# Performance work log

Hardware: AMD Instinct MI355X
Metric: run time of the kernel (lower is better)

## Reference

```python
import jax, jax.numpy as jnp
import numpy as np
import math

BN_EPS = 1e-5
BASES = [5, 4]
NH = 8    # num_heads
KD = 64   # key_dim = hidden_dim

def _bn(x, g, b, m, v):
    # eval-mode BatchNorm1d over channel dim of (B, C, L)
    s = g * jax.lax.rsqrt(v + BN_EPS)
    return (x - m[None, :, None]) * s[None, :, None] + b[None, :, None]

def _conv1x1(x, W):
    # W: (out_ch, in_ch), x: (B, C, L)
    return jnp.einsum('oc,bcl->bol', W, x)

def _dwconv3(x, W):
    # depthwise conv1d, kernel 3, pad 1. W: (C, 3)
    c = x.shape[1]
    return jax.lax.conv_general_dilated(
        x, W[:, None, :], window_strides=(1,), padding=((1, 1),),
        dimension_numbers=('NCH', 'OIH', 'NCH'), feature_group_count=c)

def _log_attn(x, base, qkW, qkg, qkb, qkm, qkv, vW, vg, vb, vm, vv,
              peW, peg, peb, pem, pev):
    b, c, w = x.shape
    hd = c // NH
    scale = KD ** -0.5
    n = int(math.log(w, base) - 1e-9) + 1
    L = base ** n
    xp = jnp.pad(x, ((0, 0), (0, 0), (0, L - w)))
    qk = _bn(_conv1x1(xp, qkW), qkg, qkb, qkm, qkv).reshape(b, NH, 2, KD, L)
    q, k = qk[:, :, 0], qk[:, :, 1]
    v0 = _bn(_conv1x1(xp, vW), vg, vb, vm, vv)  # (B, C, L)
    v2 = v0.reshape(b, NH, hd, L)
    # n sequential butterfly steps: at step i, sequence L = base^i * base * base^(n-1-i)
    for i in range(n):
        s = (base ** i, base, base ** (n - 1 - i))
        qi = q.reshape(b, NH, KD, *s)
        ki = k.reshape(b, NH, KD, *s)
        attn = jax.nn.softmax(
            jnp.einsum('bhdijk,bhdiJk->bhJijk', qi, ki) * scale, axis=4)
        v2 = jnp.einsum('bhJijk,bhdijk->bhdiJk', attn,
                        v2.reshape(b, NH, hd, *s)).reshape(b, NH, hd, L)
    v2 = v2.reshape(b, c, L)
    pe = _bn(_dwconv3(v0, peW), peg, peb, pem, pev)
    return (v2 + pe)[..., :w]

def setup_inputs():
    key = jax.random.key(0)
    ks = jax.random.split(key, 24)
    c, h, b, w = 256, 1024, 4, 3125
    return {
        'x': jax.random.normal(ks[0], (b, c, w), jnp.float32),
        'qk_W': jax.random.normal(ks[1], (2, h, c), jnp.float32) * 0.05,
        'qk_g': jax.random.normal(ks[2], (2, h), jnp.float32) * 0.1 + 1.0,
        'qk_b': jax.random.normal(ks[3], (2, h), jnp.float32) * 0.05,
        'qk_m': jax.random.normal(ks[4], (2, h), jnp.float32) * 0.05,
        'qk_v': jax.random.uniform(ks[5], (2, h), jnp.float32) + 0.5,
        'v_W': jax.random.normal(ks[6], (2, c, c), jnp.float32) * 0.05,
        'v_g': jax.random.normal(ks[7], (2, c), jnp.float32) * 0.1 + 1.0,
        'v_b': jax.random.normal(ks[8], (2, c), jnp.float32) * 0.05,
        'v_m': jax.random.normal(ks[9], (2, c), jnp.float32) * 0.05,
        'v_v': jax.random.uniform(ks[10], (2, c), jnp.float32) + 0.5,
        'pe_W': jax.random.normal(ks[11], (2, c, 3), jnp.float32) * 0.1,
        'pe_g': jax.random.normal(ks[12], (2, c), jnp.float32) * 0.1 + 1.0,
        'pe_b': jax.random.normal(ks[13], (2, c), jnp.float32) * 0.05,
        'pe_m': jax.random.normal(ks[14], (2, c), jnp.float32) * 0.05,
        'pe_v': jax.random.uniform(ks[15], (2, c), jnp.float32) + 0.5,
        'proj_W': jax.random.normal(ks[16], (c, c), jnp.float32) * 0.05,
        'proj_g': jax.random.normal(ks[17], (c,), jnp.float32) * 0.1 + 1.0,
        'proj_b': jax.random.normal(ks[18], (c,), jnp.float32) * 0.05,
        'proj_m': jax.random.normal(ks[19], (c,), jnp.float32) * 0.05,
        'proj_v': jax.random.uniform(ks[20], (c,), jnp.float32) + 0.5,
    }

def reference(x, qk_W, qk_g, qk_b, qk_m, qk_v, v_W, v_g, v_b, v_m, v_v,
              pe_W, pe_g, pe_b, pe_m, pe_v, proj_W, proj_g, proj_b,
              proj_m, proj_v):
    for idx, base in enumerate(BASES):
        x = x + _log_attn(
            x, base,
            qk_W[idx], qk_g[idx], qk_b[idx], qk_m[idx], qk_v[idx],
            v_W[idx], v_g[idx], v_b[idx], v_m[idx], v_v[idx],
            pe_W[idx], pe_g[idx], pe_b[idx], pe_m[idx], pe_v[idx])
    return _bn(_conv1x1(x, proj_W), proj_g, proj_b, proj_m, proj_v)
```

## Files before the change

kernel.cpp:

```cpp
#include <hip/hip_runtime.h>
#include <math.h>

constexpr int CW = 3125;
constexpr int CC = 256;
constexpr int CB = 4;
constexpr int NHh = 8;
constexpr int KDd = 64;
constexpr int HDd = 32;
constexpr int QROW = 64;
constexpr int VROW = 256;

typedef __attribute__((ext_vector_type(8))) short short8;
typedef __attribute__((ext_vector_type(4))) float f32x4;
typedef __attribute__((ext_vector_type(4))) unsigned int uint4v;
typedef __attribute__((ext_vector_type(2))) unsigned int uint2v;

__device__ inline unsigned short f2bf(float x) {
  unsigned int u = __float_as_uint(x);
  unsigned int r = u + 0x7FFFu + ((u >> 16) & 1u);
  return (unsigned short)(r >> 16);
}

__global__ __launch_bounds__(256) void transpose_x(const float* __restrict__ src,
                                                   float* __restrict__ dst) {
  __shared__ float sT[64][65];
  int l0 = blockIdx.x * 64, c0 = blockIdx.y * 64, bI = blockIdx.z;
  int tid = threadIdx.x;
  for (int i = tid; i < 4096; i += 256) {
    int ll = i & 63, cc = i >> 6;
    int l = l0 + ll;
    sT[cc][ll] = (l < CW) ? src[((size_t)bI * CC + c0 + cc) * CW + l] : 0.f;
  }
  __syncthreads();
  for (int i = tid; i < 4096; i += 256) {
    int cc = i & 63, ll = i >> 6;
    int l = l0 + ll;
    if (l < CW) dst[((size_t)bI * CW + l) * CC + c0 + cc] = sT[cc][ll];
  }
}

__global__ __launch_bounds__(256) void prep_w(const float* __restrict__ W0, int O0,
                                              const float* __restrict__ W1,
                                              unsigned short* __restrict__ img,
                                              int Ototal) {
  int t = blockIdx.x * 256 + threadIdx.x;
  if (t >= Ototal * 32) return;
  int o = t >> 5, ch = t & 31;
  const float* row = (o < O0) ? (W0 + (size_t)o * CC) : (W1 + (size_t)(o - O0) * CC);
  unsigned short h[8];
#pragma unroll
  for (int j = 0; j < 8; j++) h[j] = f2bf(row[ch * 8 + j]);
  uint4v v;
  v[0] = (unsigned)h[0] | ((unsigned)h[1] << 16);
  v[1] = (unsigned)h[2] | ((unsigned)h[3] << 16);
  v[2] = (unsigned)h[4] | ((unsigned)h[5] << 16);
  v[3] = (unsigned)h[6] | ((unsigned)h[7] << 16);
  int otile = o >> 7, oo = o & 127;
  int ktile = ch >> 2, kchunk = ch & 3;
  uint4v* img4 = (uint4v*)img;
  img4[((size_t)otile * 8 + ktile) * 512 + kchunk * 128 + oo] = v;
}

__global__ __launch_bounds__(256) void prep_x(const float* __restrict__ X,
                                              unsigned short* __restrict__ img, int P) {
  int ptile = blockIdx.x, cq = blockIdx.y;
  int c0 = cq * 64;
  __shared__ float sX[64][129];
  int tid = threadIdx.x;
  for (int i = tid; i < 64 * 128; i += 256) {
    int cc = i & 63, pp = i >> 6;
    int p = ptile * 128 + pp;
    sX[cc][pp] = (p < P) ? X[(size_t)p * CC + c0 + cc] : 0.f;
  }
  __syncthreads();
  uint4v* img4 = (uint4v*)img;
  for (int i = tid; i < 1024; i += 256) {
    int ch = i >> 7, pp = i & 127;
    unsigned short h[8];
#pragma unroll
    for (int j = 0; j < 8; j++) h[j] = f2bf(sX[ch * 8 + j][pp]);
    uint4v vh;
    vh[0] = (unsigned)h[0] | ((unsigned)h[1] << 16);
    vh[1] = (unsigned)h[2] | ((unsigned)h[3] << 16);
    vh[2] = (unsigned)h[4] | ((unsigned)h[5] << 16);
    vh[3] = (unsigned)h[6] | ((unsigned)h[7] << 16);
    int ktile = cq * 2 + (ch >> 2), kchunk = ch & 3;
    img4[((size_t)ptile * 8 + ktile) * 512 + kchunk * 128 + pp] = vh;
  }
}

__global__ __launch_bounds__(256, 3) void gemm_qkv(
    const unsigned short* __restrict__ Aimg, const unsigned short* __restrict__ Ximg,
    const float* __restrict__ G0, const float* __restrict__ B0,
    const float* __restrict__ M0, const float* __restrict__ V0,
    const float* __restrict__ G1, const float* __restrict__ B1,
    const float* __restrict__ M1, const float* __restrict__ V1,
    unsigned short* __restrict__ qimg, unsigned short* __restrict__ kimg,
    float* __restrict__ v0pm, int L, int P, int nOt, int ptiles) {
  int raw = blockIdx.x;
  int xcd = raw & 7;
  int t = raw >> 3;
  int ptile = (t / nOt) * 8 + xcd;
  int otile = t % nOt;
  if (ptile >= ptiles) return;
  int tid = threadIdx.x;
  int wid = tid >> 6, lane = tid & 63;
  int wr = wid >> 1, wc = wid & 1;
  int r = lane & 15, kb = lane >> 4;
  bool isV = otile >= 8;
  f32x4 acc[4][4] = {};
  const unsigned short* Ap = Aimg + (size_t)otile * 32768 + kb * 1024 + (wr * 64 + r) * 8;
  const unsigned short* Bp = Ximg + (size_t)ptile * 32768 + kb * 1024 + (wc * 64 + r) * 8;
#pragma unroll
  for (int kt = 0; kt < 8; kt++) {
    short8 a[4], b[4];
#pragma unroll
    for (int mi = 0; mi < 4; mi++) a[mi] = *(const short8*)(Ap + kt * 4096 + mi * 128);
#pragma unroll
    for (int ni = 0; ni < 4; ni++) b[ni] = *(const short8*)(Bp + kt * 4096 + ni * 128);
    if (!isV) {
#pragma unroll
      for (int mi = 0; mi < 4; mi++)
#pragma unroll
        for (int ni = 0; ni < 4; ni++)
          acc[mi][ni] = __builtin_amdgcn_mfma_f32_16x16x32_bf16(a[mi], b[ni], acc[mi][ni], 0, 0, 0);
    } else {
#pragma unroll
      for (int mi = 0; mi < 4; mi++)
#pragma unroll
        for (int ni = 0; ni < 4; ni++)
          acc[ni][mi] = __builtin_amdgcn_mfma_f32_16x16x32_bf16(b[ni], a[mi], acc[ni][mi], 0, 0, 0);
    }
  }
  int cl = lane & 15, r4 = lane >> 4;
  int p0 = ptile * 128;
  int bI0 = p0 / CW;
  int rem0 = p0 - bI0 * CW;
  if (!isV) {
#pragma unroll
    for (int mi = 0; mi < 4; mi++) {
      int obase = otile * 128 + wr * 64 + mi * 16 + r4 * 4;
      int sp = (obase >> 6) & 1;
      float qs = sp ? 1.f : 0.125f;
      float s4[4], sh4[4];
#pragma unroll
      for (int reg = 0; reg < 4; reg++) {
        int o = obase + reg;
        float sb = G0[o] * rsqrtf(V0[o] + 1e-5f);
        s4[reg] = sb * qs;
        sh4[reg] = (B0[o] - M0[o] * sb) * qs;
      }
      int nh = obase >> 7, d0 = obase & 63;
      unsigned short* dst = sp ? kimg : qimg;
#pragma unroll
      for (int ni = 0; ni < 4; ni++) {
        int off = wc * 64 + ni * 16 + cl;
        int p = p0 + off;
        if (p >= P) continue;
        int l = rem0 + off, bI = bI0;
        if (l >= CW) { l -= CW; bI++; }
        unsigned short hi[4];
#pragma unroll
        for (int reg = 0; reg < 4; reg++)
          hi[reg] = f2bf(acc[mi][ni][reg] * s4[reg] + sh4[reg]);
        uint2v hv;
        hv[0] = (unsigned)hi[0] | ((unsigned)hi[1] << 16);
        hv[1] = (unsigned)hi[2] | ((unsigned)hi[3] << 16);
        *(uint2v*)(dst + (((size_t)(bI * NHh + nh)) * L + l) * QROW + d0) = hv;
      }
    }
  } else {
#pragma unroll
    for (int mi = 0; mi < 4; mi++) {
      int oc = (otile - 8) * 128 + wr * 64 + mi * 16 + cl;
      float s = G1[oc] * rsqrtf(V1[oc] + 1e-5f);
      float sh = B1[oc] - M1[oc] * s;
#pragma unroll
      for (int ni = 0; ni < 4; ni++) {
#pragma unroll
        for (int reg = 0; reg < 4; reg++) {
          int off = wc * 64 + ni * 16 + r4 * 4 + reg;
          int p = p0 + off;
          if (p >= P) continue;
          int l = rem0 + off, bI = bI0;
          if (l >= CW) { l -= CW; bI++; }
          v0pm[((size_t)bI * L + l) * VROW + oc] = acc[ni][mi][reg] * s + sh;
        }
      }
    }
  }
}

__global__ __launch_bounds__(256, 3) void gemm_proj(
    const unsigned short* __restrict__ Aimg, const unsigned short* __restrict__ Ximg,
    const float* __restrict__ G0, const float* __restrict__ B0,
    const float* __restrict__ M0, const float* __restrict__ V0,
    float* __restrict__ out, int P, int nOt, int ptiles64) {
  int raw = blockIdx.x;
  int xcd = raw & 7;
  int t = raw >> 3;
  int p64 = (t / nOt) * 8 + xcd;
  int otile = t % nOt;
  if (p64 >= ptiles64) return;
  int tid = threadIdx.x;
  int wid = tid >> 6, lane = tid & 63;
  int wr = wid >> 1, wc = wid & 1;
  int r = lane & 15, kb = lane >> 4;
  f32x4 acc[4][2] = {};
  int ptile128 = p64 >> 1;
  int psub = (p64 & 1) * 64;
  const unsigned short* Ap = Aimg + (size_t)otile * 32768 + kb * 1024 + (wr * 64 + r) * 8;
  const unsigned short* Bp = Ximg + (size_t)ptile128 * 32768 + kb * 1024 + (psub + wc * 32 + r) * 8;
#pragma unroll
  for (int kt = 0; kt < 8; kt++) {
    short8 a[4], b[2];
#pragma unroll
    for (int mi = 0; mi < 4; mi++) a[mi] = *(const short8*)(Ap + kt * 4096 + mi * 128);
#pragma unroll
    for (int ni = 0; ni < 2; ni++) b[ni] = *(const short8*)(Bp + kt * 4096 + ni * 128);
#pragma unroll
    for (int mi = 0; mi < 4; mi++)
#pragma unroll
      for (int ni = 0; ni < 2; ni++)
        acc[mi][ni] = __builtin_amdgcn_mfma_f32_16x16x32_bf16(a[mi], b[ni], acc[mi][ni], 0, 0, 0);
  }
  int cl = lane & 15, r4 = lane >> 4;
  int p0 = p64 * 64;
  int bI0 = p0 / CW;
  int rem0 = p0 - bI0 * CW;
#pragma unroll
  for (int mi = 0; mi < 4; mi++) {
#pragma unroll
    for (int reg = 0; reg < 4; reg++) {
      int o = otile * 128 + wr * 64 + mi * 16 + r4 * 4 + reg;
      float s = G0[o] * rsqrtf(V0[o] + 1e-5f);
      float sh = B0[o] - M0[o] * s;
#pragma unroll
      for (int ni = 0; ni < 2; ni++) {
        int off = wc * 32 + ni * 16 + cl;
        int p = p0 + off;
        if (p >= P) continue;
        int l = rem0 + off, bI = bI0;
        if (l >= CW) { l -= CW; bI++; }
        out[((size_t)bI * CC + o) * CW + l] = acc[mi][ni][reg] * s + sh;
      }
    }
  }
}

__global__ __launch_bounds__(256) void pad_fill(
    const float* __restrict__ G0, const float* __restrict__ B0,
    const float* __restrict__ M0, const float* __restrict__ V0,
    const float* __restrict__ G1, const float* __restrict__ B1,
    const float* __restrict__ M1, const float* __restrict__ V1,
    unsigned short* __restrict__ qimg, unsigned short* __restrict__ kimg,
    float* __restrict__ v0pm, int L) {
  int pidx = blockIdx.x;
  int nPad = L - CW;
  int bI = pidx / nPad, l = CW + (pidx - bI * nPad);
  int tid = threadIdx.x;
  for (int o = tid; o < 1280; o += 256) {
    if (o < 1024) {
      float s = G0[o] * rsqrtf(V0[o] + 1e-5f);
      float sh = B0[o] - M0[o] * s;
      int nh = o >> 7, sp = (o >> 6) & 1, d = o & 63;
      unsigned short* dst = sp ? kimg : qimg;
      dst[(((size_t)(bI * NHh + nh)) * L + l) * QROW + d] = f2bf(sp ? sh : sh * 0.125f);
    } else {
      int oc = o - 1024;
      float s = G1[oc] * rsqrtf(V1[oc] + 1e-5f);
      float sh = B1[oc] - M1[oc] * s;
      v0pm[((size_t)bI * L + l) * VROW + oc] = sh;
    }
  }
}

template <int B, bool DO_A, bool DO_B>
__global__ __launch_bounds__(256) void attn_mfma(
    const unsigned short* __restrict__ qimg, const unsigned short* __restrict__ kimg,
    const float* __restrict__ vin, float* __restrict__ vout,
    int L, int s2, int bpb) {
  constexpr int B2 = B * B;
  constexpr int MT = (B2 + 15) / 16;
  __shared__ float S[4][256];
  int tid = threadIdx.x;
  int w = tid >> 6, lane = tid & 63;
  int gid = blockIdx.x * 4 + w;
  int bh = gid / bpb;
  int g = gid - bh * bpb;
  int hi_ = g / s2, lo_ = g - hi_ * s2;
  int base0 = hi_ * B2 * s2 + lo_;
  int cl = lane & 15, r4 = lane >> 4;
  int dd = lane & 31, half = lane >> 5;
  int bI = bh >> 3, nh = bh & 7;

  short8 kh[MT][2], qh[MT][2];
#pragma unroll
  for (int mt = 0; mt < MT; mt++) {
    int idx = mt * 16 + cl;
    if (idx > B2 - 1) idx = B2 - 1;
    size_t row = ((size_t)bh * L + base0 + idx * s2) * QROW;
#pragma unroll
    for (int kt = 0; kt < 2; kt++) {
      int dof = kt * 32 + r4 * 8;
      kh[mt][kt] = *(const short8*)(kimg + row + dof);
      qh[mt][kt] = *(const short8*)(qimg + row + dof);
    }
  }
  size_t vBase = ((size_t)bI * L + base0) * VROW + nh * HDd + dd;
  float vv[B2];
#pragma unroll
  for (int idx = 0; idx < B2; idx++) vv[idx] = vin[vBase + (size_t)(idx * s2) * VROW];

  f32x4 C[MT][MT] = {};
#pragma unroll
  for (int kt = 0; kt < 2; kt++)
#pragma unroll
    for (int mt = 0; mt < MT; mt++)
#pragma unroll
      for (int nt = 0; nt < MT; nt++)
        C[mt][nt] = __builtin_amdgcn_mfma_f32_16x16x32_bf16(kh[mt][kt], qh[nt][kt], C[mt][nt], 0, 0, 0);
#pragma unroll
  for (int mt = 0; mt < MT; mt++)
#pragma unroll
    for (int nt = 0; nt < MT; nt++)
#pragma unroll
      for (int rr = 0; rr < 4; rr++) {
        int J_idx = mt * 16 + r4 * 4 + rr;
        int j_idx = nt * 16 + cl;
        if (J_idx < B2 && j_idx < B2) {
          float val = C[mt][nt][rr];
          int Jq, bJ, jq, bj;
          if (B == 4) {
            Jq = J_idx >> 2; bJ = J_idx & 3; jq = j_idx >> 2; bj = j_idx & 3;
          } else {
            Jq = (J_idx * 205) >> 10; bJ = J_idx - Jq * 5;
            jq = (j_idx * 205) >> 10; bj = j_idx - jq * 5;
          }
          if (DO_A && bJ == bj) S[w][(bJ * B + Jq) * B + jq] = val;
          if (DO_B && Jq == jq) S[w][128 + (Jq * B + bJ) * B + bj] = val;
        }
      }
  if (DO_A) {
#pragma unroll
    for (int b = 0; b < B; b++) {
      float tmp[B];
#pragma unroll
      for (int J = 0; J < B; J++) {
        float sc[B];
#pragma unroll
        for (int j = 0; j < B; j++) sc[j] = S[w][(b * B + J) * B + j];
        float mx = sc[0];
#pragma unroll
        for (int j = 1; j < B; j++) mx = fmaxf(mx, sc[j]);
        float sum = 0.f, acc = 0.f;
#pragma unroll
        for (int j = 0; j < B; j++) {
          float e = __expf(sc[j] - mx);
          sum += e;
          acc += e * vv[j * B + b];
        }
        tmp[J] = acc / sum;
      }
#pragma unroll
      for (int J = 0; J < B; J++) vv[J * B + b] = tmp[J];
    }
  }
  if (DO_B) {
#pragma unroll
    for (int a = 0; a < B; a++) {
      float tmp[B];
#pragma unroll
      for (int J = 0; J < B; J++) {
        float sc[B];
#pragma unroll
        for (int j = 0; j < B; j++) sc[j] = S[w][128 + (a * B + J) * B + j];
        float mx = sc[0];
#pragma unroll
        for (int j = 1; j < B; j++) mx = fmaxf(mx, sc[j]);
        float sum = 0.f, acc = 0.f;
#pragma unroll
        for (int j = 0; j < B; j++) {
          float e = __expf(sc[j] - mx);
          sum += e;
          acc += e * vv[a * B + j];
        }
        tmp[J] = acc / sum;
      }
#pragma unroll
      for (int J = 0; J < B; J++) vv[a * B + J] = tmp[J];
    }
  }
#pragma unroll
  for (int idx = 0; idx < B2; idx++)
    if ((idx & 1) == half) vout[vBase + (size_t)(idx * s2) * VROW] = vv[idx];
}

template <int B, int S, bool FUSE>
__global__ __launch_bounds__(256) void attn_tri(
    const unsigned short* __restrict__ qimg, const unsigned short* __restrict__ kimg,
    const float* __restrict__ vin, float* __restrict__ vout,
    int L, int nblk,
    const float* __restrict__ peW, const float* __restrict__ Gp,
    const float* __restrict__ Bp2, const float* __restrict__ Mp,
    const float* __restrict__ Vp, const float* __restrict__ v0pm,
    float* __restrict__ xcur) {
  constexpr int B2 = B * B;
  constexpr int B3 = B * B * B;
  constexpr int NT = (B3 + 15) / 16;
  constexpr int MTW = (NT + 3) / 4;
  __shared__ float slab[3 * B2 * B * B];
  __shared__ float sv[B3 * 33];
  int tid = threadIdx.x;
  int w = tid >> 6, lane = tid & 63;
  int bid = blockIdx.x;
  int bh = bid / nblk;
  int blk = bid - bh * nblk;
  int hi = blk / S, lo = blk - hi * S;
  int base0 = hi * B3 * S + lo;
  int bI = bh >> 3, nh = bh & 7;
  int cl = lane & 15, r4 = lane >> 4;

  for (int t = tid; t < B3 * 32; t += 256) {
    int c = t & 31, idx = t >> 5;
    sv[idx * 33 + c] = vin[((size_t)bI * L + base0 + idx * S) * VROW + nh * HDd + c];
  }

  short8 kh[MTW][2], qh[NT][2];
#pragma unroll
  for (int m = 0; m < MTW; m++) {
    int idx = (w * MTW + m) * 16 + cl;
    if (idx > B3 - 1) idx = B3 - 1;
    size_t row = ((size_t)bh * L + base0 + idx * S) * QROW;
#pragma unroll
    for (int kt = 0; kt < 2; kt++)
      kh[m][kt] = *(const short8*)(kimg + row + kt * 32 + r4 * 8);
  }
#pragma unroll
  for (int nt = 0; nt < NT; nt++) {
    int idx = nt * 16 + cl;
    if (idx > B3 - 1) idx = B3 - 1;
    size_t row = ((size_t)bh * L + base0 + idx * S) * QROW;
#pragma unroll
    for (int kt = 0; kt < 2; kt++)
      qh[nt][kt] = *(const short8*)(qimg + row + kt * 32 + r4 * 8);
  }
  f32x4 C[MTW][NT] = {};
#pragma unroll
  for (int kt = 0; kt < 2; kt++)
#pragma unroll
    for (int m = 0; m < MTW; m++)
#pragma unroll
      for (int nt = 0; nt < NT; nt++)
        C[m][nt] = __builtin_amdgcn_mfma_f32_16x16x32_bf16(kh[m][kt], qh[nt][kt], C[m][nt], 0, 0, 0);
#pragma unroll
  for (int m = 0; m < MTW; m++)
#pragma unroll
    for (int nt = 0; nt < NT; nt++)
#pragma unroll
      for (int rr = 0; rr < 4; rr++) {
        int J = (w * MTW + m) * 16 + r4 * 4 + rr;
        int j = nt * 16 + cl;
        if (J < B3 && j < B3) {
          float val = C[m][nt][rr];
          int A2 = J / B2, Jr = J - A2 * B2, A1 = Jr / B, A0 = Jr - A1 * B;
          int a2 = j / B2, jr = j - a2 * B2, a1 = jr / B, a0 = jr - a1 * B;
          if (A1 == a1 && A0 == a0) slab[((0 * B2 + (a1 * B + a0)) * B + A2) * B + a2] = val;
          if (A2 == a2 && A0 == a0) slab[((1 * B2 + (a2 * B + a0)) * B + A1) * B + a1] = val;
          if (A2 == a2 && A1 == a1) slab[((2 * B2 + (a2 * B + a1)) * B + A0) * B + a0] = val;
        }
      }
  __syncthreads();
  if (tid < 3 * B2) {
    float* bw = &slab[tid * B * B];
#pragma unroll
    for (int J = 0; J < B; J++) {
      float mx = bw[J * B];
#pragma unroll
      for (int j = 1; j < B; j++) mx = fmaxf(mx, bw[J * B + j]);
      float sum = 0.f;
      float e[B];
#pragma unroll
      for (int j = 0; j < B; j++) {
        e[j] = __expf(bw[J * B + j] - mx);
        sum += e[j];
      }
      float inv = 1.f / sum;
#pragma unroll
      for (int j = 0; j < B; j++) bw[J * B + j] = e[j] * inv;
    }
  }
  __syncthreads();
  int c = tid & 31, slot = tid >> 5;
  for (int lvl = 0; lvl < 3; lvl++) {
    for (int g = slot; g < B2; g += 8) {
      int ghi = g / B, glo = g - ghi * B;
      const float* wrow = &slab[(lvl * B2 + g) * B * B];
      float vvals[B], outs[B];
#pragma unroll
      for (int j = 0; j < B; j++) {
        int pid = (lvl == 0) ? (j * B2 + g) : (lvl == 1) ? (ghi * B2 + j * B + glo) : (g * B + j);
        vvals[j] = sv[pid * 33 + c];
      }
#pragma unroll
      for (int J = 0; J < B; J++) {
        float a = 0.f;
#pragma unroll
        for (int j = 0; j < B; j++) a += wrow[J * B + j] * vvals[j];
        outs[J] = a;
      }
#pragma unroll
      for (int J = 0; J < B; J++) {
        int pid = (lvl == 0) ? (J * B2 + g) : (lvl == 1) ? (ghi * B2 + J * B + glo) : (g * B + J);
        sv[pid * 33 + c] = outs[J];
      }
    }
    __syncthreads();
  }
  if (!FUSE) {
    for (int t = tid; t < B3 * 32; t += 256) {
      int c2 = t & 31, idx = t >> 5;
      vout[((size_t)bI * L + base0 + idx * S) * VROW + nh * HDd + c2] = sv[idx * 33 + c2];
    }
  } else {
    int ch = nh * HDd + c;
    float pw0 = peW[ch * 3 + 0], pw1 = peW[ch * 3 + 1], pw2 = peW[ch * 3 + 2];
    float s = Gp[ch] * rsqrtf(Vp[ch] + 1e-5f);
    float sh = Bp2[ch] - Mp[ch] * s;
    for (int idx = slot; idx < B3; idx += 8) {
      int l = base0 + idx;
      if (l >= CW) continue;
      size_t row = ((size_t)bI * L + l) * VROW + ch;
      float left = (l > 0) ? v0pm[row - VROW] : 0.f;
      float mid = v0pm[row];
      float right = (l + 1 < L) ? v0pm[row + VROW] : 0.f;
      float pe = (left * pw0 + mid * pw1 + right * pw2) * s + sh;
      xcur[((size_t)bI * CW + l) * CC + ch] += sv[idx * 33 + c] + pe;
    }
  }
}

extern "C" void kernel_launch(void* const* d_in, const int* in_sizes, int n_in,
                              void* d_out, int out_size, void* d_ws, size_t ws_size,
                              hipStream_t stream) {
  const float* x = (const float*)d_in[0];
  const float* qk_W = (const float*)d_in[1];
  const float* qk_g = (const float*)d_in[2];
  const float* qk_b = (const float*)d_in[3];
  const float* qk_m = (const float*)d_in[4];
  const float* qk_v = (const float*)d_in[5];
  const float* v_W = (const float*)d_in[6];
  const float* v_g = (const float*)d_in[7];
  const float* v_b = (const float*)d_in[8];
  const float* v_m = (const float*)d_in[9];
  const float* v_v = (const float*)d_in[10];
  const float* pe_W = (const float*)d_in[11];
  const float* pe_g = (const float*)d_in[12];
  const float* pe_b = (const float*)d_in[13];
  const float* pe_m = (const float*)d_in[14];
  const float* pe_v = (const float*)d_in[15];
  const float* proj_W = (const float*)d_in[16];
  const float* proj_g = (const float*)d_in[17];
  const float* proj_b = (const float*)d_in[18];
  const float* proj_m = (const float*)d_in[19];
  const float* proj_v = (const float*)d_in[20];

  char* ws = (char*)d_ws;
  size_t off = 0;
  auto alloc = [&](size_t bytes) {
    char* p = ws + off;
    off += (bytes + 255) & ~(size_t)255;
    return (void*)p;
  };
  const int Lmax = 4096;
  const int P = CB * CW;
  const int ptiles = (P + 127) / 128;
  float* xcur = (float*)alloc((size_t)CB * CW * CC * 4);
  unsigned short* qimg = (unsigned short*)alloc((size_t)CB * NHh * Lmax * QROW * 2);
  unsigned short* kimg = (unsigned short*)alloc((size_t)CB * NHh * Lmax * QROW * 2);
  float* v0pm = (float*)alloc((size_t)CB * Lmax * VROW * 4);
  float* vA = (float*)alloc((size_t)CB * Lmax * VROW * 4);
  unsigned short* Wimg = (unsigned short*)alloc((size_t)10 * 8 * 8192 * 2);
  unsigned short* Ximg = (unsigned short*)vA;
  (void)ws_size;

  {
    dim3 gt((CW + 63) / 64, 4, CB);
    transpose_x<<<gt, 256, 0, stream>>>(x, xcur);
  }

  const int pgroups8 = (ptiles + 7) / 8;
  const int ptiles64 = (P + 63) / 64;
  const int pg64 = (ptiles64 + 7) / 8;
  const int bases[2] = {5, 4};
  const int Ls[2] = {3125, 4096};
  for (int blk = 0; blk < 2; blk++) {
    int L = Ls[blk];
    prep_w<<<(1280 * 32 + 255) / 256, 256, 0, stream>>>(
        qk_W + (size_t)blk * 1024 * CC, 1024, v_W + (size_t)blk * CC * CC, Wimg, 1280);
    dim3 gx(ptiles, 4);
    prep_x<<<gx, 256, 0, stream>>>(xcur, Ximg, P);
    gemm_qkv<<<8 * pgroups8 * 10, 256, 0, stream>>>(
        Wimg, Ximg, qk_g + blk * 1024, qk_b + blk * 1024, qk_m + blk * 1024,
        qk_v + blk * 1024, v_g + blk * CC, v_b + blk * CC, v_m + blk * CC,
        v_v + blk * CC, qimg, kimg, v0pm, L, P, 10, ptiles);
    if (L > CW) {
      pad_fill<<<CB * (L - CW), 256, 0, stream>>>(
          qk_g + blk * 1024, qk_b + blk * 1024, qk_m + blk * 1024, qk_v + blk * 1024,
          v_g + blk * CC, v_b + blk * CC, v_m + blk * CC, v_v + blk * CC,
          qimg, kimg, v0pm, L);
    }

    const float* peWb = pe_W + (size_t)blk * CC * 3;
    const float* peG = pe_g + blk * CC;
    const float* peB = pe_b + blk * CC;
    const float* peM = pe_m + blk * CC;
    const float* peV = pe_v + blk * CC;
    if (bases[blk] == 5) {
      int bpb = L / 25;
      attn_mfma<5, true, true><<<(CB * NHh * bpb) / 4, 256, 0, stream>>>(
          qimg, kimg, v0pm, vA, L, 125, bpb);
      int nblk = L / 125;
      attn_tri<5, 1, true><<<CB * NHh * nblk, 256, 0, stream>>>(
          qimg, kimg, vA, nullptr, L, nblk, peWb, peG, peB, peM, peV, v0pm, xcur);
    } else {
      int nblk = L / 64;
      attn_tri<4, 64, false><<<CB * NHh * nblk, 256, 0, stream>>>(
          qimg, kimg, v0pm, vA, L, nblk, nullptr, nullptr, nullptr, nullptr,
          nullptr, nullptr, nullptr);
      attn_tri<4, 1, true><<<CB * NHh * nblk, 256, 0, stream>>>(
          qimg, kimg, vA, nullptr, L, nblk, peWb, peG, peB, peM, peV, v0pm, xcur);
    }
  }
  {
    prep_w<<<(256 * 32 + 255) / 256, 256, 0, stream>>>(proj_W, 256, nullptr, Wimg, 256);
    dim3 gx(ptiles, 4);
    prep_x<<<gx, 256, 0, stream>>>(xcur, Ximg, P);
    gemm_proj<<<8 * pg64 * 2, 256, 0, stream>>>(
        Wimg, Ximg, proj_g, proj_b, proj_m, proj_v, (float*)d_out, P, 2, ptiles64);
  }
}
```

Baseline: 266.1 us.

## Split attn_tri head channels across two blocks and hoist index decode

```diff
diff --git a/kernel.cpp b/kernel.cpp
--- a/kernel.cpp
+++ b/kernel.cpp
@@ -409,21 +409,24 @@
   constexpr int B3 = B * B * B;
   constexpr int NT = (B3 + 15) / 16;
   constexpr int MTW = (NT + 3) / 4;
+  constexpr int NCH = 16;
   __shared__ float slab[3 * B2 * B * B];
-  __shared__ float sv[B3 * 33];
+  __shared__ float sv[B3 * (NCH + 1)];
   int tid = threadIdx.x;
   int w = tid >> 6, lane = tid & 63;
-  int bid = blockIdx.x;
-  int bh = bid / nblk;
-  int blk = bid - bh * nblk;
+  int unit = blockIdx.x >> 1;
+  int csel = blockIdx.x & 1;
+  int bh = unit / nblk;
+  int blk = unit - bh * nblk;
   int hi = blk / S, lo = blk - hi * S;
   int base0 = hi * B3 * S + lo;
   int bI = bh >> 3, nh = bh & 7;
   int cl = lane & 15, r4 = lane >> 4;
-
-  for (int t = tid; t < B3 * 32; t += 256) {
-    int c = t & 31, idx = t >> 5;
-    sv[idx * 33 + c] = vin[((size_t)bI * L + base0 + idx * S) * VROW + nh * HDd + c];
+  int cbase = nh * HDd + csel * NCH;
+
+  for (int t = tid; t < B3 * NCH; t += 256) {
+    int c = t & (NCH - 1), idx = t >> 4;
+    sv[idx * (NCH + 1) + c] = vin[((size_t)bI * L + base0 + idx * S) * VROW + cbase + c];
   }
 
   short8 kh[MTW][2], qh[NT][2];
@@ -453,23 +456,42 @@
 #pragma unroll
       for (int nt = 0; nt < NT; nt++)
         C[m][nt] = __builtin_amdgcn_mfma_f32_16x16x32_bf16(kh[m][kt], qh[nt][kt], C[m][nt], 0, 0, 0);
+  int jd2[NT], jd1[NT], jd0[NT];
+  bool jok[NT];
+#pragma unroll
+  for (int nt = 0; nt < NT; nt++) {
+    int j = nt * 16 + cl;
+    jok[nt] = (j < B3);
+    if (j > B3 - 1) j = B3 - 1;
+    jd2[nt] = j / B2;
+    int jr = j - jd2[nt] * B2;
+    jd1[nt] = jr / B;
+    jd0[nt] = jr - jd1[nt] * B;
+  }
 #pragma unroll
   for (int m = 0; m < MTW; m++)
 #pragma unroll
-    for (int nt = 0; nt < NT; nt++)
-#pragma unroll
-      for (int rr = 0; rr < 4; rr++) {
-        int J = (w * MTW + m) * 16 + r4 * 4 + rr;
-        int j = nt * 16 + cl;
-        if (J < B3 && j < B3) {
+    for (int rr = 0; rr < 4; rr++) {
+      int J = (w * MTW + m) * 16 + r4 * 4 + rr;
+      bool Jok = (J < B3);
+      int Jc = Jok ? J : (B3 - 1);
+      int A2 = Jc / B2;
+      int Jr = Jc - A2 * B2;
+      int A1 = Jr / B;
+      int A0 = Jr - A1 * B;
+#pragma unroll
+      for (int nt = 0; nt < NT; nt++) {
+        if (Jok && jok[nt]) {
           float val = C[m][nt][rr];
-          int A2 = J / B2, Jr = J - A2 * B2, A1 = Jr / B, A0 = Jr - A1 * B;
-          int a2 = j / B2, jr = j - a2 * B2, a1 = jr / B, a0 = jr - a1 * B;
-          if (A1 == a1 && A0 == a0) slab[((0 * B2 + (a1 * B + a0)) * B + A2) * B + a2] = val;
-          if (A2 == a2 && A0 == a0) slab[((1 * B2 + (a2 * B + a0)) * B + A1) * B + a1] = val;
-          if (A2 == a2 && A1 == a1) slab[((2 * B2 + (a2 * B + a1)) * B + A0) * B + a0] = val;
+          if (A1 == jd1[nt] && A0 == jd0[nt])
+            slab[((0 * B2 + (jd1[nt] * B + jd0[nt])) * B + A2) * B + jd2[nt]] = val;
+          if (A2 == jd2[nt] && A0 == jd0[nt])
+            slab[((1 * B2 + (jd2[nt] * B + jd0[nt])) * B + A1) * B + jd1[nt]] = val;
+          if (A2 == jd2[nt] && A1 == jd1[nt])
+            slab[((2 * B2 + (jd2[nt] * B + jd1[nt])) * B + A0) * B + jd0[nt]] = val;
         }
       }
+    }
   __syncthreads();
   if (tid < 3 * B2) {
     float* bw = &slab[tid * B * B];
@@ -491,16 +513,16 @@
     }
   }
   __syncthreads();
-  int c = tid & 31, slot = tid >> 5;
+  int c = tid & (NCH - 1), slot = tid >> 4;
   for (int lvl = 0; lvl < 3; lvl++) {
-    for (int g = slot; g < B2; g += 8) {
+    for (int g = slot; g < B2; g += 16) {
       int ghi = g / B, glo = g - ghi * B;
       const float* wrow = &slab[(lvl * B2 + g) * B * B];
       float vvals[B], outs[B];
 #pragma unroll
       for (int j = 0; j < B; j++) {
         int pid = (lvl == 0) ? (j * B2 + g) : (lvl == 1) ? (ghi * B2 + j * B + glo) : (g * B + j);
-        vvals[j] = sv[pid * 33 + c];
+        vvals[j] = sv[pid * (NCH + 1) + c];
       }
 #pragma unroll
       for (int J = 0; J < B; J++) {
@@ -512,22 +534,22 @@
 #pragma unroll
       for (int J = 0; J < B; J++) {
         int pid = (lvl == 0) ? (J * B2 + g) : (lvl == 1) ? (ghi * B2 + J * B + glo) : (g * B + J);
-        sv[pid * 33 + c] = outs[J];
+        sv[pid * (NCH + 1) + c] = outs[J];
       }
     }
     __syncthreads();
   }
   if (!FUSE) {
-    for (int t = tid; t < B3 * 32; t += 256) {
-      int c2 = t & 31, idx = t >> 5;
-      vout[((size_t)bI * L + base0 + idx * S) * VROW + nh * HDd + c2] = sv[idx * 33 + c2];
+    for (int t = tid; t < B3 * NCH; t += 256) {
+      int c2 = t & (NCH - 1), idx = t >> 4;
+      vout[((size_t)bI * L + base0 + idx * S) * VROW + cbase + c2] = sv[idx * (NCH + 1) + c2];
     }
   } else {
-    int ch = nh * HDd + c;
+    int ch = cbase + c;
     float pw0 = peW[ch * 3 + 0], pw1 = peW[ch * 3 + 1], pw2 = peW[ch * 3 + 2];
     float s = Gp[ch] * rsqrtf(Vp[ch] + 1e-5f);
     float sh = Bp2[ch] - Mp[ch] * s;
-    for (int idx = slot; idx < B3; idx += 8) {
+    for (int idx = slot; idx < B3; idx += 16) {
       int l = base0 + idx;
       if (l >= CW) continue;
       size_t row = ((size_t)bI * L + l) * VROW + ch;
@@ -535,7 +557,7 @@
       float mid = v0pm[row];
       float right = (l + 1 < L) ? v0pm[row + VROW] : 0.f;
       float pe = (left * pw0 + mid * pw1 + right * pw2) * s + sh;
-      xcur[((size_t)bI * CW + l) * CC + ch] += sv[idx * 33 + c] + pe;
+      xcur[((size_t)bI * CW + l) * CC + ch] += sv[idx * (NCH + 1) + c] + pe;
     }
   }
 }
@@ -621,14 +643,14 @@
       attn_mfma<5, true, true><<<(CB * NHh * bpb) / 4, 256, 0, stream>>>(
           qimg, kimg, v0pm, vA, L, 125, bpb);
       int nblk = L / 125;
-      attn_tri<5, 1, true><<<CB * NHh * nblk, 256, 0, stream>>>(
+      attn_tri<5, 1, true><<<CB * NHh * nblk * 2, 256, 0, stream>>>(
           qimg, kimg, vA, nullptr, L, nblk, peWb, peG, peB, peM, peV, v0pm, xcur);
     } else {
       int nblk = L / 64;
-      attn_tri<4, 64, false><<<CB * NHh * nblk, 256, 0, stream>>>(
+      attn_tri<4, 64, false><<<CB * NHh * nblk * 2, 256, 0, stream>>>(
           qimg, kimg, v0pm, vA, L, nblk, nullptr, nullptr, nullptr, nullptr,
           nullptr, nullptr, nullptr);
-      attn_tri<4, 1, true><<<CB * NHh * nblk, 256, 0, stream>>>(
+      attn_tri<4, 1, true><<<CB * NHh * nblk * 2, 256, 0, stream>>>(
           qimg, kimg, vA, nullptr, L, nblk, peWb, peG, peB, peM, peV, v0pm, xcur);
     }
   }
```

New measurement: 296.3 us. 11.4% more time.
